# Optimization experiments

Measured on AMD Instinct MI355X. Metric: run time of the kernel, lower is better.

The kernel has to match this reference:

```python
import jax, jax.numpy as jnp
import numpy as np

V, N, C, DIM, DSPAN, H = 200000, 16384, 16, 300, 512, 150


def setup_inputs() -> dict:
    key = jax.random.key(0)
    ks = jax.random.split(key, 6)
    span_vecs = jax.random.normal(ks[0], (1, N, DSPAN), jnp.float32)
    candidates = jax.random.randint(ks[1], (1, N, C), 0, V)
    # binary candidate mask; guarantee every span has at least one candidate
    mask = (jax.random.uniform(ks[2], (1, N, C)) > 0.3).astype(jnp.float32)
    mask = mask.at[..., 0].set(1.0)
    embed_table = jax.random.normal(ks[3], (V, DIM), jnp.float32) * 0.1
    W1 = jax.random.normal(ks[4], (DSPAN + DIM, H), jnp.float32) * (1.0 / np.sqrt(DSPAN + DIM))
    b1 = jnp.zeros((H,), jnp.float32)
    W2 = jax.random.normal(ks[5], (H, 1), jnp.float32) * (1.0 / np.sqrt(H))
    b2 = jnp.zeros((1,), jnp.float32)
    return dict(span_vecs=span_vecs, candidates=candidates, mask_candidates=mask,
                embed_table=embed_table, W1=W1, b1=b1, W2=W2, b2=b2)


def reference(span_vecs, candidates, mask_candidates, embed_table, W1, b1, W2, b2):
    # gather candidate entity embeddings: [N, C, dim]
    cand_emb = embed_table[candidates[0]]
    sv = span_vecs[0]                                  # [N, Dspan]
    n, c = cand_emb.shape[0], cand_emb.shape[1]
    spans_exp = jnp.broadcast_to(sv[:, None, :], (n, c, sv.shape[-1]))
    ment = jnp.concatenate([spans_exp, cand_emb], axis=-1)  # [N, C, Dspan+dim]
    # 2-layer attention MLP scorer
    h = jax.nn.relu(ment @ W1 + b1)                    # [N, C, H]
    scores = (h @ W2 + b2)[..., 0]                     # [N, C]
    # masked softmax over candidates (log(0) = -inf masks out)
    scores = jax.nn.softmax(scores + jnp.log(mask_candidates[0]), axis=-1)
    # weighted sum of candidate embeddings
    weighted = jnp.einsum('ncd,nc->nd', cand_emb, scores)   # [N, dim]
    # pad span_vecs with dim zeros then scatter weighted into last dim slots
    # == concat since every span has candidates here
    out = jnp.concatenate([sv, weighted], axis=-1)[None]    # [1, N, Dspan+dim]
    return out
```

## Files before the change

kernel.cpp:

```cpp
#include <hip/hip_runtime.h>
#include <hip/hip_bf16.h>
#include <math.h>

#define NSPANS 16384
#define CC     16
#define DIM    300
#define DSPAN  512
#define HH     150
#define HP     160
#define DMENT  812
#define KP     320
#define BSTR   328

typedef short bf16x8 __attribute__((ext_vector_type(8)));
typedef float f32x4  __attribute__((ext_vector_type(4)));

__device__ __forceinline__ unsigned short f2bf(float f) {
    union { float f; unsigned int u; } v; v.f = f;
    unsigned int r = (v.u + 0x7FFFu + ((v.u >> 16) & 1u)) >> 16;
    return (unsigned short)r;
}

__global__ __launch_bounds__(256) void k0_prep(const float* __restrict__ W1,
                                               unsigned short* __restrict__ Wt) {
    int idx = blockIdx.x * 256 + threadIdx.x;
    int n = idx / KP, k = idx - n * KP;
    float v = (n < HH && k < DIM) ? W1[(size_t)(DSPAN + k) * HH + n] : 0.f;
    Wt[idx] = f2bf(v);
}

__global__ __launch_bounds__(256) void k1_span(const float* __restrict__ sv,
                                               const float* __restrict__ W1,
                                               const float* __restrict__ b1,
                                               float* __restrict__ out) {
    const int b  = blockIdx.x;
    const int t  = threadIdx.x;
    const int n0 = b * 32;

    __shared__ float svc_t[32][36];
    __shared__ float w1c[32][HP];

    #pragma unroll
    for (int i = 0; i < 16; ++i) {
        int idx4 = t + i * 256;
        int r = idx4 >> 7, c4 = idx4 & 127;
        float4 v = *(const float4*)(sv + (size_t)(n0 + r) * DSPAN + c4 * 4);
        *(float4*)(out + (size_t)(n0 + r) * DMENT + c4 * 4) = v;
    }

    const int tc = t & 31;
    const int tr = t >> 5;
    const int j0 = tc * 5;
    const int r0 = tr * 4;

    float acc[4][5];
    #pragma unroll
    for (int i = 0; i < 4; ++i)
        #pragma unroll
        for (int j = 0; j < 5; ++j) acc[i][j] = 0.f;

    for (int k0 = 0; k0 < DSPAN; k0 += 32) {
        __syncthreads();
        {
            int r = t >> 3, c4 = t & 7;
            float4 v = *(const float4*)(sv + (size_t)(n0 + r) * DSPAN + k0 + c4 * 4);
            svc_t[c4 * 4 + 0][r] = v.x;
            svc_t[c4 * 4 + 1][r] = v.y;
            svc_t[c4 * 4 + 2][r] = v.z;
            svc_t[c4 * 4 + 3][r] = v.w;
        }
        #pragma unroll
        for (int i = 0; i < 20; ++i) {
            int idx = t + i * 256;
            int k = idx / HP, j = idx - (idx / HP) * HP;
            w1c[k][j] = (j < HH) ? W1[(size_t)(k0 + k) * HH + j] : 0.f;
        }
        __syncthreads();
        #pragma unroll
        for (int kk = 0; kk < 32; ++kk) {
            float4 a4 = *(const float4*)&svc_t[kk][r0];
            #pragma unroll
            for (int j = 0; j < 5; ++j) {
                float w = w1c[kk][j0 + j];
                acc[0][j] += a4.x * w;
                acc[1][j] += a4.y * w;
                acc[2][j] += a4.z * w;
                acc[3][j] += a4.w * w;
            }
        }
    }

    #pragma unroll
    for (int i = 0; i < 4; ++i)
        #pragma unroll
        for (int j = 0; j < 5; ++j) {
            int jj = j0 + j;
            if (jj < HH)
                out[(size_t)(n0 + r0 + i) * DMENT + DSPAN + jj] = acc[i][j] + b1[jj];
        }
}

__global__ __launch_bounds__(512) void k2_mfma(const int*   __restrict__ cand,
                                               const float* __restrict__ mask,
                                               const float* __restrict__ emb,
                                               const unsigned short* __restrict__ Wt,
                                               const float* __restrict__ W2,
                                               float*       __restrict__ out) {
    const int b  = blockIdx.x;
    const int t  = threadIdx.x;
    const int n0 = b * 8;
    const int w  = t >> 6;
    const int l  = t & 63;
    const int sp = l & 15;
    const int g  = l >> 4;

    __shared__ unsigned short B_lds[160][BSTR];
    __shared__ float hsL[8][HP];
    __shared__ float w2L[HP];
    __shared__ int   candL[128];
    __shared__ float maskL[128];
    __shared__ float pL[8][16];

    if (t < 128) {
        candL[t] = cand[n0 * CC + t];
        maskL[t] = mask[n0 * CC + t];
    }
    for (int idx = t; idx < 8 * HP; idx += 512) {
        int s = idx / HP, j = idx - s * HP;
        hsL[s][j] = (j < HH) ? out[(size_t)(n0 + s) * DMENT + DSPAN + j] : 0.f;
    }
    if (t < HP) w2L[t] = (t < HH) ? W2[t] : 0.f;
    for (int idx = t; idx < 6400; idx += 512) {
        int row = idx / 40, seg = idx - row * 40;
        uint4 v = *(const uint4*)(Wt + (size_t)row * KP + seg * 8);
        *(uint4*)&B_lds[row][seg * 8] = v;
    }
    __syncthreads();

    const float* asrc = emb + (size_t)candL[w * 16 + sp] * DIM;

    float4 a[10][2];
    #pragma unroll
    for (int kt = 0; kt < 10; ++kt)
        #pragma unroll
        for (int h = 0; h < 2; ++h) {
            int kb = kt * 32 + g * 8 + h * 4;
            a[kt][h] = (kb < DIM) ? *(const float4*)(asrc + kb)
                                  : make_float4(0.f, 0.f, 0.f, 0.f);
        }

    f32x4 acc[10];
    #pragma unroll
    for (int nt = 0; nt < 10; ++nt) acc[nt] = 0.f;

    #pragma unroll
    for (int kt = 0; kt < 10; ++kt) {
        union { uint4 u; bf16x8 h; } cv;
        cv.u.x = f2bf(a[kt][0].x) | ((unsigned)f2bf(a[kt][0].y) << 16);
        cv.u.y = f2bf(a[kt][0].z) | ((unsigned)f2bf(a[kt][0].w) << 16);
        cv.u.z = f2bf(a[kt][1].x) | ((unsigned)f2bf(a[kt][1].y) << 16);
        cv.u.w = f2bf(a[kt][1].z) | ((unsigned)f2bf(a[kt][1].w) << 16);
        bf16x8 af = cv.h;
        const int koff = kt * 32 + g * 8;
        #pragma unroll
        for (int nt = 0; nt < 10; ++nt) {
            bf16x8 bfr = *(const bf16x8*)&B_lds[nt * 16 + sp][koff];
            acc[nt] = __builtin_amdgcn_mfma_f32_16x16x32_bf16(af, bfr, acc[nt], 0, 0, 0);
        }
    }

    float s0 = 0.f, s1 = 0.f, s2 = 0.f, s3 = 0.f;
    #pragma unroll
    for (int nt = 0; nt < 10; ++nt) {
        int col = nt * 16 + sp;
        float hb  = hsL[w][col];
        float w2v = w2L[col];
        s0 += fmaxf(acc[nt][0] + hb, 0.f) * w2v;
        s1 += fmaxf(acc[nt][1] + hb, 0.f) * w2v;
        s2 += fmaxf(acc[nt][2] + hb, 0.f) * w2v;
        s3 += fmaxf(acc[nt][3] + hb, 0.f) * w2v;
    }
    #pragma unroll
    for (int m = 1; m < 16; m <<= 1) {
        s0 += __shfl_xor(s0, m, 64);
        s1 += __shfl_xor(s1, m, 64);
        s2 += __shfl_xor(s2, m, 64);
        s3 += __shfl_xor(s3, m, 64);
    }

    float v0 = (maskL[w * 16 + g * 4 + 0] > 0.f) ? s0 : -INFINITY;
    float v1 = (maskL[w * 16 + g * 4 + 1] > 0.f) ? s1 : -INFINITY;
    float v2 = (maskL[w * 16 + g * 4 + 2] > 0.f) ? s2 : -INFINITY;
    float v3 = (maskL[w * 16 + g * 4 + 3] > 0.f) ? s3 : -INFINITY;
    float mx = fmaxf(fmaxf(v0, v1), fmaxf(v2, v3));
    mx = fmaxf(mx, __shfl_xor(mx, 16, 64));
    mx = fmaxf(mx, __shfl_xor(mx, 32, 64));
    float e0 = expf(v0 - mx), e1 = expf(v1 - mx), e2 = expf(v2 - mx), e3 = expf(v3 - mx);
    float sm = (e0 + e1) + (e2 + e3);
    sm += __shfl_xor(sm, 16, 64);
    sm += __shfl_xor(sm, 32, 64);
    if (sp == 0) {
        pL[w][g * 4 + 0] = e0 / sm;
        pL[w][g * 4 + 1] = e1 / sm;
        pL[w][g * 4 + 2] = e2 / sm;
        pL[w][g * 4 + 3] = e3 / sm;
    }
    __syncthreads();

    float pr[16];
    const float* rp[16];
    #pragma unroll
    for (int c = 0; c < CC; ++c) {
        pr[c] = pL[w][c];
        rp[c] = emb + (size_t)candL[w * 16 + c] * DIM;
    }
    for (int q = l; q < 75; q += 64) {
        float4 acc4 = make_float4(0.f, 0.f, 0.f, 0.f);
        #pragma unroll
        for (int c = 0; c < CC; ++c) {
            float p = pr[c];
            float4 v = *(const float4*)(rp[c] + q * 4);
            acc4.x += p * v.x; acc4.y += p * v.y; acc4.z += p * v.z; acc4.w += p * v.w;
        }
        *(float4*)(out + (size_t)(n0 + w) * DMENT + DSPAN + q * 4) = acc4;
    }
}

extern "C" void kernel_launch(void* const* d_in, const int* in_sizes, int n_in,
                              void* d_out, int out_size, void* d_ws, size_t ws_size,
                              hipStream_t stream) {
    const float* sv   = (const float*)d_in[0];
    const int*   cand = (const int*)d_in[1];
    const float* mask = (const float*)d_in[2];
    const float* emb  = (const float*)d_in[3];
    const float* W1   = (const float*)d_in[4];
    const float* b1   = (const float*)d_in[5];
    const float* W2   = (const float*)d_in[6];
    float* out = (float*)d_out;
    unsigned short* Wt = (unsigned short*)d_ws;

    k0_prep<<<(HP * KP) / 256, 256, 0, stream>>>(W1, Wt);
    k1_span<<<NSPANS / 32, 256, 0, stream>>>(sv, W1, b1, out);
    k2_mfma<<<NSPANS / 8, 512, 0, stream>>>(cand, mask, emb, Wt, W2, out);
}
```

Measured before the change: 628.1 us.

## Split-K the span GEMM and widen the MFMA kernel to 16 spans per block

k1_span now uses 512 threads split into two teams, each covering half of the K dimension, and combines the partial sums through shared memory. k2_mfma processes 16 spans per 1024-thread block, so each staged copy of the bf16 W1 tile in LDS serves twice as many spans and each CU holds more waves to hide gather latency. The embedding A-operand loads become a two-stage register prefetch instead of loading all tiles up front, which lowers register pressure. The block barrier before the weighted sum is removed because pL is only read back by the wave that wrote it; this relies on wave-local LDS ordering.

```diff
diff --git a/kernel.cpp b/kernel.cpp
--- a/kernel.cpp
+++ b/kernel.cpp
@@ -29,29 +29,33 @@
     Wt[idx] = f2bf(v);
 }
 
-__global__ __launch_bounds__(256) void k1_span(const float* __restrict__ sv,
+__global__ __launch_bounds__(512) void k1_span(const float* __restrict__ sv,
                                                const float* __restrict__ W1,
                                                const float* __restrict__ b1,
                                                float* __restrict__ out) {
     const int b  = blockIdx.x;
     const int t  = threadIdx.x;
     const int n0 = b * 32;
-
-    __shared__ float svc_t[32][36];
-    __shared__ float w1c[32][HP];
-
-    #pragma unroll
-    for (int i = 0; i < 16; ++i) {
-        int idx4 = t + i * 256;
+    const int team = t >> 8;
+    const int u    = t & 255;
+
+    __shared__ float svc_t[2][32][36];
+    __shared__ float w1c[2][32][HP];
+    __shared__ float partial[32][HP];
+
+    #pragma unroll
+    for (int i = 0; i < 8; ++i) {
+        int idx4 = t + i * 512;
         int r = idx4 >> 7, c4 = idx4 & 127;
         float4 v = *(const float4*)(sv + (size_t)(n0 + r) * DSPAN + c4 * 4);
         *(float4*)(out + (size_t)(n0 + r) * DMENT + c4 * 4) = v;
     }
 
-    const int tc = t & 31;
-    const int tr = t >> 5;
+    const int tc = u & 31;
+    const int tr = u >> 5;
     const int j0 = tc * 5;
     const int r0 = tr * 4;
+    const int kbase = team * 256;
 
     float acc[4][5];
     #pragma unroll
@@ -59,29 +63,29 @@
         #pragma unroll
         for (int j = 0; j < 5; ++j) acc[i][j] = 0.f;
 
-    for (int k0 = 0; k0 < DSPAN; k0 += 32) {
+    for (int k0 = 0; k0 < 256; k0 += 32) {
         __syncthreads();
         {
-            int r = t >> 3, c4 = t & 7;
-            float4 v = *(const float4*)(sv + (size_t)(n0 + r) * DSPAN + k0 + c4 * 4);
-            svc_t[c4 * 4 + 0][r] = v.x;
-            svc_t[c4 * 4 + 1][r] = v.y;
-            svc_t[c4 * 4 + 2][r] = v.z;
-            svc_t[c4 * 4 + 3][r] = v.w;
+            int r = u >> 3, c4 = u & 7;
+            float4 v = *(const float4*)(sv + (size_t)(n0 + r) * DSPAN + kbase + k0 + c4 * 4);
+            svc_t[team][c4 * 4 + 0][r] = v.x;
+            svc_t[team][c4 * 4 + 1][r] = v.y;
+            svc_t[team][c4 * 4 + 2][r] = v.z;
+            svc_t[team][c4 * 4 + 3][r] = v.w;
         }
         #pragma unroll
         for (int i = 0; i < 20; ++i) {
-            int idx = t + i * 256;
+            int idx = u + i * 256;
             int k = idx / HP, j = idx - (idx / HP) * HP;
-            w1c[k][j] = (j < HH) ? W1[(size_t)(k0 + k) * HH + j] : 0.f;
+            w1c[team][k][j] = (j < HH) ? W1[(size_t)(kbase + k0 + k) * HH + j] : 0.f;
         }
         __syncthreads();
         #pragma unroll
         for (int kk = 0; kk < 32; ++kk) {
-            float4 a4 = *(const float4*)&svc_t[kk][r0];
+            float4 a4 = *(const float4*)&svc_t[team][kk][r0];
             #pragma unroll
             for (int j = 0; j < 5; ++j) {
-                float w = w1c[kk][j0 + j];
+                float w = w1c[team][kk][j0 + j];
                 acc[0][j] += a4.x * w;
                 acc[1][j] += a4.y * w;
                 acc[2][j] += a4.z * w;
@@ -90,48 +94,59 @@
         }
     }
 
-    #pragma unroll
-    for (int i = 0; i < 4; ++i)
-        #pragma unroll
-        for (int j = 0; j < 5; ++j) {
-            int jj = j0 + j;
-            if (jj < HH)
-                out[(size_t)(n0 + r0 + i) * DMENT + DSPAN + jj] = acc[i][j] + b1[jj];
-        }
-}
-
-__global__ __launch_bounds__(512) void k2_mfma(const int*   __restrict__ cand,
-                                               const float* __restrict__ mask,
-                                               const float* __restrict__ emb,
-                                               const unsigned short* __restrict__ Wt,
-                                               const float* __restrict__ W2,
-                                               float*       __restrict__ out) {
+    if (team == 1) {
+        #pragma unroll
+        for (int i = 0; i < 4; ++i)
+            #pragma unroll
+            for (int j = 0; j < 5; ++j)
+                partial[r0 + i][j0 + j] = acc[i][j];
+    }
+    __syncthreads();
+    if (team == 0) {
+        #pragma unroll
+        for (int i = 0; i < 4; ++i)
+            #pragma unroll
+            for (int j = 0; j < 5; ++j) {
+                int jj = j0 + j;
+                if (jj < HH)
+                    out[(size_t)(n0 + r0 + i) * DMENT + DSPAN + jj] =
+                        (acc[i][j] + partial[r0 + i][jj]) + b1[jj];
+            }
+    }
+}
+
+__global__ __launch_bounds__(1024) void k2_mfma(const int*   __restrict__ cand,
+                                                const float* __restrict__ mask,
+                                                const float* __restrict__ emb,
+                                                const unsigned short* __restrict__ Wt,
+                                                const float* __restrict__ W2,
+                                                float*       __restrict__ out) {
     const int b  = blockIdx.x;
     const int t  = threadIdx.x;
-    const int n0 = b * 8;
+    const int n0 = b * 16;
     const int w  = t >> 6;
     const int l  = t & 63;
     const int sp = l & 15;
     const int g  = l >> 4;
 
     __shared__ unsigned short B_lds[160][BSTR];
-    __shared__ float hsL[8][HP];
+    __shared__ float hsL[16][HP];
     __shared__ float w2L[HP];
-    __shared__ int   candL[128];
-    __shared__ float maskL[128];
-    __shared__ float pL[8][16];
-
-    if (t < 128) {
+    __shared__ int   candL[256];
+    __shared__ float maskL[256];
+    __shared__ float pL[16][16];
+
+    if (t < 256) {
         candL[t] = cand[n0 * CC + t];
         maskL[t] = mask[n0 * CC + t];
     }
-    for (int idx = t; idx < 8 * HP; idx += 512) {
+    for (int idx = t; idx < 16 * HP; idx += 1024) {
         int s = idx / HP, j = idx - s * HP;
         hsL[s][j] = (j < HH) ? out[(size_t)(n0 + s) * DMENT + DSPAN + j] : 0.f;
     }
     if (t < HP) w2L[t] = (t < HH) ? W2[t] : 0.f;
-    for (int idx = t; idx < 6400; idx += 512) {
-        int row = idx / 40, seg = idx - row * 40;
+    for (int idx = t; idx < 6400; idx += 1024) {
+        int row = idx / 40, seg = idx - (idx / 40) * 40;
         uint4 v = *(const uint4*)(Wt + (size_t)row * KP + seg * 8);
         *(uint4*)&B_lds[row][seg * 8] = v;
     }
@@ -139,15 +154,12 @@
 
     const float* asrc = emb + (size_t)candL[w * 16 + sp] * DIM;
 
-    float4 a[10][2];
-    #pragma unroll
-    for (int kt = 0; kt < 10; ++kt)
-        #pragma unroll
-        for (int h = 0; h < 2; ++h) {
-            int kb = kt * 32 + g * 8 + h * 4;
-            a[kt][h] = (kb < DIM) ? *(const float4*)(asrc + kb)
-                                  : make_float4(0.f, 0.f, 0.f, 0.f);
-        }
+    float4 abuf[2][2];
+    #pragma unroll
+    for (int h = 0; h < 2; ++h) {
+        abuf[0][h] = *(const float4*)(asrc + g * 8 + h * 4);
+        abuf[1][h] = *(const float4*)(asrc + 32 + g * 8 + h * 4);
+    }
 
     f32x4 acc[10];
     #pragma unroll
@@ -155,12 +167,21 @@
 
     #pragma unroll
     for (int kt = 0; kt < 10; ++kt) {
-        union { uint4 u; bf16x8 h; } cv;
-        cv.u.x = f2bf(a[kt][0].x) | ((unsigned)f2bf(a[kt][0].y) << 16);
-        cv.u.y = f2bf(a[kt][0].z) | ((unsigned)f2bf(a[kt][0].w) << 16);
-        cv.u.z = f2bf(a[kt][1].x) | ((unsigned)f2bf(a[kt][1].y) << 16);
-        cv.u.w = f2bf(a[kt][1].z) | ((unsigned)f2bf(a[kt][1].w) << 16);
-        bf16x8 af = cv.h;
+        const int cur = kt & 1;
+        union { uint4 u; bf16x8 h8; } cv;
+        cv.u.x = f2bf(abuf[cur][0].x) | ((unsigned)f2bf(abuf[cur][0].y) << 16);
+        cv.u.y = f2bf(abuf[cur][0].z) | ((unsigned)f2bf(abuf[cur][0].w) << 16);
+        cv.u.z = f2bf(abuf[cur][1].x) | ((unsigned)f2bf(abuf[cur][1].y) << 16);
+        cv.u.w = f2bf(abuf[cur][1].z) | ((unsigned)f2bf(abuf[cur][1].w) << 16);
+        bf16x8 af = cv.h8;
+        if (kt + 2 < 10) {
+            #pragma unroll
+            for (int h = 0; h < 2; ++h) {
+                int kb = (kt + 2) * 32 + g * 8 + h * 4;
+                abuf[cur][h] = (kb < DIM) ? *(const float4*)(asrc + kb)
+                                          : make_float4(0.f, 0.f, 0.f, 0.f);
+            }
+        }
         const int koff = kt * 32 + g * 8;
         #pragma unroll
         for (int nt = 0; nt < 10; ++nt) {
@@ -205,24 +226,17 @@
         pL[w][g * 4 + 2] = e2 / sm;
         pL[w][g * 4 + 3] = e3 / sm;
     }
-    __syncthreads();
-
-    float pr[16];
-    const float* rp[16];
-    #pragma unroll
-    for (int c = 0; c < CC; ++c) {
-        pr[c] = pL[w][c];
-        rp[c] = emb + (size_t)candL[w * 16 + c] * DIM;
-    }
+
     for (int q = l; q < 75; q += 64) {
-        float4 acc4 = make_float4(0.f, 0.f, 0.f, 0.f);
+        float4 a4 = make_float4(0.f, 0.f, 0.f, 0.f);
         #pragma unroll
         for (int c = 0; c < CC; ++c) {
-            float p = pr[c];
-            float4 v = *(const float4*)(rp[c] + q * 4);
-            acc4.x += p * v.x; acc4.y += p * v.y; acc4.z += p * v.z; acc4.w += p * v.w;
-        }
-        *(float4*)(out + (size_t)(n0 + w) * DMENT + DSPAN + q * 4) = acc4;
+            float p = pL[w][c];
+            const float* rp = emb + (size_t)candL[w * 16 + c] * DIM;
+            float4 v = *(const float4*)(rp + q * 4);
+            a4.x += p * v.x; a4.y += p * v.y; a4.z += p * v.z; a4.w += p * v.w;
+        }
+        *(float4*)(out + (size_t)(n0 + w) * DMENT + DSPAN + q * 4) = a4;
     }
 }
 
@@ -240,6 +254,6 @@
     unsigned short* Wt = (unsigned short*)d_ws;
 
     k0_prep<<<(HP * KP) / 256, 256, 0, stream>>>(W1, Wt);
-    k1_span<<<NSPANS / 32, 256, 0, stream>>>(sv, W1, b1, out);
-    k2_mfma<<<NSPANS / 8, 512, 0, stream>>>(cand, mask, emb, Wt, W2, out);
-}
+    k1_span<<<NSPANS / 32, 512, 0, stream>>>(sv, W1, b1, out);
+    k2_mfma<<<NSPANS / 16, 1024, 0, stream>>>(cand, mask, emb, Wt, W2, out);
+}
```

Measured after the change: 586.3 us. -6.7%, faster.
